# Optimization experiments

Measured on AMD Instinct MI355X. Metric: run time of the kernel, lower is better.

## Reference

```python
import jax, jax.numpy as jnp
import numpy as np

B, S, H, NH = 8, 1024, 1024, 16
D = H // NH          # attention_hidden_size = 64
V = S                # v_size must equal seq_len (mask broadcast)


def setup_inputs() -> dict:
    key = jax.random.key(0)
    ks = jax.random.split(key, 9)
    s = 0.02
    return {
        "q": jax.random.normal(ks[0], (B, S, H), jnp.float32),
        "k": jax.random.normal(ks[1], (B, S, H), jnp.float32),
        "v": jax.random.normal(ks[2], (B, S, H), jnp.float32),
        # per-head Q/K projections, stacked over heads: (NH, H, D)
        "Wq": jax.random.normal(ks[3], (NH, H, D), jnp.float32) * s,
        "bq": jax.random.normal(ks[4], (NH, D), jnp.float32) * s,
        "Wk": jax.random.normal(ks[5], (NH, H, D), jnp.float32) * s,
        "bk": jax.random.normal(ks[6], (NH, D), jnp.float32) * s,
        # shared V projection hidden -> v_size
        "Wv": jax.random.normal(ks[7], (H, V), jnp.float32) * s,
        "bv": jax.random.normal(ks[8], (V,), jnp.float32) * s,
    }


def reference(q, k, v, Wq, bq, Wk, bk, Wv, bv):
    d = Wq.shape[-1]
    scale = d ** (-0.5)
    # per-head projections, heads vectorized into leading axis n
    qh = jnp.einsum('bsh,nhd->nbsd', q, Wq) + bq[:, None, None, :]
    kh = jnp.einsum('bth,nhd->nbtd', k, Wk) + bk[:, None, None, :]
    vv = jnp.einsum('bth,hv->btv', v, Wv) + bv          # shared V: (B,S,V)
    seq = q.shape[1]
    mask = jnp.triu(jnp.full((seq, seq), -jnp.inf, dtype=q.dtype), 1)
    scores = jnp.einsum('nbsd,nbtd->nbst', qh, kh) * scale + mask
    p = jax.nn.softmax(scores, axis=-1)                  # (NH,B,S,S)
    # matmul against shared V then mean over heads (== stack + mean)
    out = jnp.einsum('nbst,btv->nbsv', p, vv).mean(axis=0)
    return out
```

## Files before the change

### kernel.cpp

```cpp
#include <hip/hip_runtime.h>


#define NHEAD 16
#define BATCH 8
#define SEQ   1024
#define HID   1024
#define DHEAD 64

typedef _Float16 f16;
typedef _Float16 f16x4 __attribute__((ext_vector_type(4)));
typedef _Float16 f16x8 __attribute__((ext_vector_type(8)));
typedef float    f32x4 __attribute__((ext_vector_type(4)));

__device__ __forceinline__ f32x4 mfma16(f16x8 a, f16x8 b, f32x4 c) {
  return __builtin_amdgcn_mfma_f32_16x16x32_f16(a, b, c, 0, 0, 0);
}

__device__ __forceinline__ void gload16(const f16* g, f16* l) {
  __builtin_amdgcn_global_load_lds(
      (const __attribute__((address_space(1))) void*)g,
      (__attribute__((address_space(3))) void*)l, 16, 0, 0);
}

__device__ __forceinline__ void stage_swz(const f16* __restrict__ g, int ldg,
                                          f16* lds, int nch, int tid) {
  for (int idx = tid; idx < nch; idx += 256) {
    int row = idx >> 3, c16 = idx & 7;
    int sc = c16 ^ (row & 7);
    gload16(g + (size_t)row * ldg + sc * 8, lds + (size_t)(idx & ~63) * 8);
  }
}

__device__ __forceinline__ f16x8 lds_frag(const f16* lds, int row, int c16) {
  int sc = c16 ^ (row & 7);
  return *(const f16x8*)&lds[row * 64 + sc * 8];
}


__global__ __launch_bounds__(256) void conv3(
    const float* __restrict__ q, const float* __restrict__ k,
    const float* __restrict__ v, f16* __restrict__ dq, f16* __restrict__ dk,
    f16* __restrict__ dv) {
  const float* src = blockIdx.z == 0 ? q : blockIdx.z == 1 ? k : v;
  f16* dst = blockIdx.z == 0 ? dq : blockIdx.z == 1 ? dk : dv;
  int i = (blockIdx.x * 256 + threadIdx.x) * 4;
  float4 f = *(const float4*)(src + i);
  f16x4 o = { (f16)f.x, (f16)f.y, (f16)f.z, (f16)f.w };
  *(f16x4*)(dst + i) = o;
}

__global__ __launch_bounds__(256) void tconv2(
    const float* __restrict__ s0, const float* __restrict__ s1,
    f16* __restrict__ d0, f16* __restrict__ d1, int R, int C, int half) {
  int z = blockIdx.z;
  const float* src; f16* dst;
  if (z < half) { src = s0 + (size_t)z * R * C; dst = d0 + (size_t)z * R * C; }
  else { src = s1 + (size_t)(z - half) * R * C; dst = d1 + (size_t)(z - half) * R * C; }
  const int c0 = blockIdx.x * 64, r0 = blockIdx.y * 64;
  __shared__ f16 t[64][72];
  const int tid = threadIdx.x;
#pragma unroll
  for (int i = 0; i < 4; i++) {
    int chunk = tid + i * 256;
    int row = chunk >> 4, c4 = chunk & 15;
    float4 f = *(const float4*)&src[(size_t)(r0 + row) * C + c0 + c4 * 4];
    f16x4 h = { (f16)f.x, (f16)f.y, (f16)f.z, (f16)f.w };
    *(f16x4*)&t[row][c4 * 4] = h;
  }
  __syncthreads();
  const int cc = tid >> 2, q = tid & 3;
  f16 tmp[16];
#pragma unroll
  for (int j = 0; j < 16; j++) tmp[j] = t[q * 16 + j][cc];
  *(f16x8*)&dst[(size_t)(c0 + cc) * R + r0 + q * 16] = *(f16x8*)&tmp[0];
  *(f16x8*)&dst[(size_t)(c0 + cc) * R + r0 + q * 16 + 8] = *(f16x8*)&tmp[8];
}


__device__ __forceinline__ void gemm_core(
    const f16* __restrict__ A, const f16* __restrict__ Bt, int K, int Kend,
    int row0, int col0, f16* la, f16* lb, int tid, f32x4 (&acc)[4][4]) {
  const int lane = tid & 63;
  const int wr = (tid >> 6) >> 1, wc = (tid >> 6) & 1;
  for (int k0 = 0; k0 < Kend; k0 += 64) {
    __syncthreads();
    stage_swz(A + (size_t)row0 * K + k0, K, la, 1024, tid);
    stage_swz(Bt + (size_t)col0 * K + k0, K, lb, 1024, tid);
    __syncthreads();
#pragma unroll
    for (int ks = 0; ks < 2; ks++) {
      f16x8 af[4], bfr[4];
#pragma unroll
      for (int mi = 0; mi < 4; mi++)
        af[mi] = lds_frag(la, wr * 64 + mi * 16 + (lane & 15), ks * 4 + (lane >> 4));
#pragma unroll
      for (int ni = 0; ni < 4; ni++)
        bfr[ni] = lds_frag(lb, wc * 64 + ni * 16 + (lane & 15), ks * 4 + (lane >> 4));
#pragma unroll
      for (int mi = 0; mi < 4; mi++)
#pragma unroll
        for (int ni = 0; ni < 4; ni++)
          acc[mi][ni] = mfma16(af[mi], bfr[ni], acc[mi][ni]);
    }
  }
}


__global__ __launch_bounds__(256) void proj_gemm(
    const f16* __restrict__ A0, const f16* __restrict__ A1,
    const f16* __restrict__ Bt0, const f16* __restrict__ Bt1,
    const float* __restrict__ bias0, const float* __restrict__ bias1,
    f16* __restrict__ C0, f16* __restrict__ C1) {
  const int which = blockIdx.z;
  const f16* A = which ? A1 : A0;
  const f16* Bt = which ? Bt1 : Bt0;
  const float* bias = which ? bias1 : bias0;
  f16* C = which ? C1 : C0;
  __shared__ alignas(16) f16 la[128 * 64];
  __shared__ alignas(16) f16 lb[128 * 64];
  const int tid = threadIdx.x, lane = tid & 63;
  const int wr = (tid >> 6) >> 1, wc = (tid >> 6) & 1;
  const int row0 = blockIdx.x * 128, col0 = blockIdx.y * 128;
  f32x4 acc[4][4];
#pragma unroll
  for (int i = 0; i < 4; i++)
#pragma unroll
    for (int j = 0; j < 4; j++) acc[i][j] = (f32x4){0.f, 0.f, 0.f, 0.f};
  gemm_core(A, Bt, HID, HID, row0, col0, la, lb, tid, acc);
#pragma unroll
  for (int mi = 0; mi < 4; mi++)
#pragma unroll
    for (int ni = 0; ni < 4; ni++)
#pragma unroll
      for (int r = 0; r < 4; r++) {
        int m = row0 + wr * 64 + mi * 16 + ((lane >> 4) << 2) + r;
        int j = col0 + wc * 64 + ni * 16 + (lane & 15);
        float val = acc[mi][ni][r] + bias[j];
        int bb = m >> 10, s = m & 1023, hn = j >> 6, d = j & 63;
        C[(((size_t)hn * BATCH + bb) * SEQ + s) * DHEAD + d] = (f16)val;
      }
}


__global__ __launch_bounds__(256) void vv_gemm(
    const f16* __restrict__ A, const f16* __restrict__ Bt,
    const float* __restrict__ bias, f16* __restrict__ C) {
  __shared__ alignas(16) f16 la[128 * 64];
  __shared__ alignas(16) f16 lb[128 * 64];
  const int tid = threadIdx.x, lane = tid & 63;
  const int wr = (tid >> 6) >> 1, wc = (tid >> 6) & 1;
  const int row0 = blockIdx.x * 128, col0 = blockIdx.y * 128;
  f32x4 acc[4][4];
#pragma unroll
  for (int i = 0; i < 4; i++)
#pragma unroll
    for (int j = 0; j < 4; j++) acc[i][j] = (f32x4){0.f, 0.f, 0.f, 0.f};
  gemm_core(A, Bt, HID, HID, row0, col0, la, lb, tid, acc);
#pragma unroll
  for (int mi = 0; mi < 4; mi++)
#pragma unroll
    for (int ni = 0; ni < 4; ni++)
#pragma unroll
      for (int r = 0; r < 4; r++) {
        int m = row0 + wr * 64 + mi * 16 + ((lane >> 4) << 2) + r;
        int j = col0 + wc * 64 + ni * 16 + (lane & 15);
        float val = acc[mi][ni][r] + bias[m];
        int bb = j >> 10, t = j & 1023;
        C[((size_t)bb * SEQ + m) * SEQ + t] = (f16)val;
      }
}


__global__ __launch_bounds__(256) void attn_stats(
    const f16* __restrict__ QH, const f16* __restrict__ KH,
    float* __restrict__ madj_ws) {
  const int flat = blockIdx.x;
  const int sb = 15 - (flat >> 7);
  const int nb = flat & 127;
  const int n = nb >> 3, b = nb & 7;
  const int s0 = sb * 64;
  const f16* qh = QH + ((size_t)n * BATCH + b) * SEQ * DHEAD;
  const f16* kh = KH + ((size_t)n * BATCH + b) * SEQ * DHEAD;

  const int tid = threadIdx.x, lane = tid & 63, wave = tid >> 6;
  const int lr = lane & 15;
  const int qg = lane >> 4;
  const int ch = qg << 3;

  f16x8 aq[4][2];
#pragma unroll
  for (int fi = 0; fi < 4; fi++) {
    const f16* qp = qh + (size_t)(s0 + fi * 16 + lr) * 64 + ch;
    aq[fi][0] = *(const f16x8*)qp;
    aq[fi][1] = *(const f16x8*)(qp + 32);
  }

  const float sl2e = 0.125f * 1.44269504088896f;
  float l_p[16];
#pragma unroll
  for (int i = 0; i < 16; i++) l_p[i] = 0.f;

  const int nt = (sb + 1) * 4;
  const int dstart = sb * 4;
  const int njw = (nt - wave + 3) >> 2;
  const f16* kp = kh + (size_t)lr * 64 + ch;

  f16x8 kA0, kA1, kB0, kB1;

#define LDK(jj, X0, X1) { const f16* p_ = kp + (size_t)(jj) * 1024; \
    X0 = *(const f16x8*)p_; X1 = *(const f16x8*)(p_ + 32); }

#define COMP(jj, X0, X1) { \
    f32x4 c_[4]; \
    _Pragma("unroll") for (int fi = 0; fi < 4; fi++) { \
      f32x4 cc = (f32x4){0.f, 0.f, 0.f, 0.f}; \
      cc = mfma16(aq[fi][0], X0, cc); cc = mfma16(aq[fi][1], X1, cc); \
      c_[fi] = cc; } \
    if ((jj) < dstart) { \
      _Pragma("unroll") for (int fi = 0; fi < 4; fi++) \
        _Pragma("unroll") for (int r = 0; r < 4; r++) \
          l_p[fi * 4 + r] += exp2f(c_[fi][r] * sl2e); \
    } else { \
      int tg_ = (jj) * 16 + lr; \
      _Pragma("unroll") for (int fi = 0; fi < 4; fi++) \
        _Pragma("unroll") for (int r = 0; r < 4; r++) { \
          int sg_ = s0 + fi * 16 + qg * 4 + r; \
          l_p[fi * 4 + r] += (tg_ <= sg_) ? exp2f(c_[fi][r] * sl2e) : 0.f; } } }

  LDK(wave, kA0, kA1);
  int idx = 0;
  for (; idx + 2 <= njw; idx += 2) {
    LDK(wave + (idx + 1) * 4, kB0, kB1);
    COMP(wave + idx * 4, kA0, kA1);
    if (idx + 2 < njw) LDK(wave + (idx + 2) * 4, kA0, kA1);
    COMP(wave + (idx + 1) * 4, kB0, kB1);
  }
  if (idx < njw) COMP(wave + idx * 4, kA0, kA1);
#undef LDK
#undef COMP

  __shared__ float lds_l[4][64];
#pragma unroll
  for (int i = 0; i < 16; i++) {
    float l = l_p[i];
    l += __shfl_xor(l, 1); l += __shfl_xor(l, 2);
    l += __shfl_xor(l, 4); l += __shfl_xor(l, 8);
    if (lr == 0) lds_l[wave][(i >> 2) * 16 + qg * 4 + (i & 3)] = l;
  }
  __syncthreads();
  if (tid < 64) {
    float l = lds_l[0][tid] + lds_l[1][tid] + lds_l[2][tid] + lds_l[3][tid];
    madj_ws[((size_t)n * BATCH + b) * SEQ + s0 + tid] = -__log2f(l) - 4.0f;
  }
}


__global__ __launch_bounds__(256) void pbar_gemm(
    const f16* __restrict__ QH, const f16* __restrict__ KH,
    const float* __restrict__ madj_ws, f16* __restrict__ pp) {
  int ti = blockIdx.x, rb = 0, cb = 0;
  {
    int t = ti;
#pragma unroll
    for (int r = 0; r < 8; ++r) {
      if (t <= r) { rb = r; cb = t; break; }
      t -= r + 1;
    }
  }
  const int r0 = rb * 128, c0 = cb * 128;
  const int y = blockIdx.y;
  const int b = y >> 1, g = y & 1;
  const int n0 = g * 8;
  const bool diag = (rb == cb);

  __shared__ alignas(16) f16 la[128 * 64];
  __shared__ alignas(16) f16 lb[128 * 64];

  const int tid = threadIdx.x, lane = tid & 63;
  const int wr = (tid >> 6) >> 1, wc = (tid >> 6) & 1;
  const int lr = lane & 15, qg = lane >> 4;
  const float sl2e = 0.125f * 1.44269504088896f;

  f32x4 pacc[4][4];
#pragma unroll
  for (int i = 0; i < 4; i++)
#pragma unroll
    for (int j = 0; j < 4; j++) pacc[i][j] = (f32x4){0.f, 0.f, 0.f, 0.f};

  for (int h = 0; h < 8; ++h) {
    const int n = n0 + h;
    const f16* qh = QH + ((size_t)n * BATCH + b) * SEQ * DHEAD;
    const f16* kh = KH + ((size_t)n * BATCH + b) * SEQ * DHEAD;

    __syncthreads();
    stage_swz(qh + (size_t)r0 * 64, 64, la, 1024, tid);
    stage_swz(kh + (size_t)c0 * 64, 64, lb, 1024, tid);
    __syncthreads();

    f32x4 acc[4][4];
#pragma unroll
    for (int i = 0; i < 4; i++)
#pragma unroll
      for (int j = 0; j < 4; j++) acc[i][j] = (f32x4){0.f, 0.f, 0.f, 0.f};

#pragma unroll
    for (int ks = 0; ks < 2; ks++) {
      f16x8 af[4], bfr[4];
#pragma unroll
      for (int mi = 0; mi < 4; mi++)
        af[mi] = lds_frag(la, wr * 64 + mi * 16 + lr, ks * 4 + qg);
#pragma unroll
      for (int ni = 0; ni < 4; ni++)
        bfr[ni] = lds_frag(lb, wc * 64 + ni * 16 + lr, ks * 4 + qg);
#pragma unroll
      for (int mi = 0; mi < 4; mi++)
#pragma unroll
        for (int ni = 0; ni < 4; ni++)
          acc[mi][ni] = mfma16(af[mi], bfr[ni], acc[mi][ni]);
    }

    const float* mb = madj_ws + ((size_t)n * BATCH + b) * SEQ + r0 +
                      wr * 64 + qg * 4;
#pragma unroll
    for (int mi = 0; mi < 4; mi++) {
      float4 m4 = *(const float4*)(mb + mi * 16);
      float ma[4] = {m4.x, m4.y, m4.z, m4.w};
#pragma unroll
      for (int ni = 0; ni < 4; ni++) {
        int tg = c0 + wc * 64 + ni * 16 + lr;
#pragma unroll
        for (int r = 0; r < 4; r++) {
          float p = exp2f(fmaf(acc[mi][ni][r], sl2e, ma[r]));
          if (diag) {
            int sg = r0 + wr * 64 + mi * 16 + qg * 4 + r;
            p = (tg <= sg) ? p : 0.f;
          }
          pacc[mi][ni][r] += p;
        }
      }
    }
  }

  f16* out = pp + ((size_t)g * BATCH + b) * SEQ * SEQ;
#pragma unroll
  for (int mi = 0; mi < 4; mi++)
#pragma unroll
    for (int ni = 0; ni < 4; ni++)
#pragma unroll
      for (int r = 0; r < 4; r++) {
        int m = r0 + wr * 64 + mi * 16 + qg * 4 + r;
        int j = c0 + wc * 64 + ni * 16 + lr;
        out[(size_t)m * SEQ + j] = (f16)pacc[mi][ni][r];
      }
}


__global__ __launch_bounds__(256) void pv_gemm(
    const f16* __restrict__ pp, const f16* __restrict__ vvT,
    float* __restrict__ out) {
  const int b = blockIdx.z;
  const size_t GS = (size_t)BATCH * SEQ * SEQ;
  const f16* A0 = pp + (size_t)b * SEQ * SEQ;
  const f16* A1 = pp + GS + (size_t)b * SEQ * SEQ;
  const f16* Bt = vvT + (size_t)b * SEQ * SEQ;
  __shared__ alignas(16) f16 la0[128 * 64];
  __shared__ alignas(16) f16 la1[128 * 64];
  __shared__ alignas(16) f16 lb[128 * 64];
  const int tid = threadIdx.x, lane = tid & 63;
  const int wr = (tid >> 6) >> 1, wc = (tid >> 6) & 1;
  const int row0 = blockIdx.x * 128, col0 = blockIdx.y * 128;
  const int Kend = (row0 + 128 < SEQ) ? row0 + 128 : SEQ;

  f32x4 acc[4][4];
#pragma unroll
  for (int i = 0; i < 4; i++)
#pragma unroll
    for (int j = 0; j < 4; j++) acc[i][j] = (f32x4){0.f, 0.f, 0.f, 0.f};

  for (int k0 = 0; k0 < Kend; k0 += 64) {
    __syncthreads();
    stage_swz(A0 + (size_t)row0 * SEQ + k0, SEQ, la0, 1024, tid);
    stage_swz(A1 + (size_t)row0 * SEQ + k0, SEQ, la1, 1024, tid);
    stage_swz(Bt + (size_t)col0 * SEQ + k0, SEQ, lb, 1024, tid);
    __syncthreads();
#pragma unroll
    for (int ks = 0; ks < 2; ks++) {
      f16x8 a0[4], a1[4], bfr[4];
#pragma unroll
      for (int mi = 0; mi < 4; mi++) {
        a0[mi] = lds_frag(la0, wr * 64 + mi * 16 + (lane & 15), ks * 4 + (lane >> 4));
        a1[mi] = lds_frag(la1, wr * 64 + mi * 16 + (lane & 15), ks * 4 + (lane >> 4));
      }
#pragma unroll
      for (int ni = 0; ni < 4; ni++)
        bfr[ni] = lds_frag(lb, wc * 64 + ni * 16 + (lane & 15), ks * 4 + (lane >> 4));
#pragma unroll
      for (int mi = 0; mi < 4; mi++)
#pragma unroll
        for (int ni = 0; ni < 4; ni++) {
          acc[mi][ni] = mfma16(a0[mi], bfr[ni], acc[mi][ni]);
          acc[mi][ni] = mfma16(a1[mi], bfr[ni], acc[mi][ni]);
        }
    }
  }

#pragma unroll
  for (int mi = 0; mi < 4; mi++)
#pragma unroll
    for (int ni = 0; ni < 4; ni++)
#pragma unroll
      for (int r = 0; r < 4; r++) {
        int m = row0 + wr * 64 + mi * 16 + ((lane >> 4) << 2) + r;
        int j = col0 + wc * 64 + ni * 16 + (lane & 15);
        out[(size_t)b * SEQ * SEQ + (size_t)m * SEQ + j] = acc[mi][ni][r];
      }
}


extern "C" void kernel_launch(void* const* d_in, const int* in_sizes, int n_in,
                              void* d_out, int out_size, void* d_ws, size_t ws_size,
                              hipStream_t stream) {
  (void)in_sizes; (void)n_in; (void)out_size; (void)ws_size;
  const float* q  = (const float*)d_in[0];
  const float* k  = (const float*)d_in[1];
  const float* v  = (const float*)d_in[2];
  const float* Wq = (const float*)d_in[3];
  const float* bq = (const float*)d_in[4];
  const float* Wk = (const float*)d_in[5];
  const float* bk = (const float*)d_in[6];
  const float* Wv = (const float*)d_in[7];
  const float* bv = (const float*)d_in[8];
  float* out = (float*)d_out;

  const size_t EL  = (size_t)BATCH * SEQ * HID;
  const size_t WEL = (size_t)NHEAD * HID * DHEAD;

  char* ws = (char*)d_ws;
  f16* qbf = (f16*)ws;  ws += EL * 2;
  f16* kbf = (f16*)ws;  ws += EL * 2;
  f16* vbf = (f16*)ws;  ws += EL * 2;
  f16* WqT = (f16*)ws;  ws += WEL * 2;
  f16* WkT = (f16*)ws;  ws += WEL * 2;
  f16* WvT = (f16*)ws;  ws += WEL * 2;
  f16* QHb = (f16*)ws;  ws += EL * 2;
  f16* KHb = (f16*)ws;  ws += EL * 2;
  f16* vvT = (f16*)ws;  ws += EL * 2;
  float* madj_ws = (float*)ws; ws += (size_t)NHEAD * BATCH * SEQ * 4;
  f16* pp = qbf;

  conv3<<<dim3(8192, 1, 3), 256, 0, stream>>>(q, k, v, qbf, kbf, vbf);
  tconv2<<<dim3(1, 16, 32), 256, 0, stream>>>(Wq, Wk, WqT, WkT, 1024, 64, 16);
  tconv2<<<dim3(16, 16, 1), 256, 0, stream>>>(Wv, Wv, WvT, WvT, 1024, 1024, 1);

  proj_gemm<<<dim3(64, 8, 2), 256, 0, stream>>>(qbf, kbf, WqT, WkT, bq, bk,
                                                QHb, KHb);
  vv_gemm<<<dim3(8, 64, 1), 256, 0, stream>>>(WvT, vbf, bv, vvT);

  attn_stats<<<dim3(2048, 1, 1), 256, 0, stream>>>(QHb, KHb, madj_ws);
  pbar_gemm<<<dim3(36, 16, 1), 256, 0, stream>>>(QHb, KHb, madj_ws, pp);
  pv_gemm<<<dim3(8, 8, 8), 256, 0, stream>>>(pp, vvT, out);
}
```

Measured before the change: 238.3 us.

## Double-buffer head tiles in pbar_gemm and remap blocks across XCDs

Gives pbar_gemm two LDS buffers for the Q/K head tiles so the load for the next head is issued while the current head's MFMAs and exp run. This removes one barrier per head and hides global-load latency. It also hoists the madj loads ahead of the compute and launches a flat 1D grid whose index is permuted so that consecutive blocks (same batch and group) land on the same XCD for L2 reuse. In exchange LDS use doubles to 64KB per block, which may lower occupancy.

```diff
diff --git a/kernel.cpp b/kernel.cpp
--- a/kernel.cpp
+++ b/kernel.cpp
@@ -258,9 +258,12 @@
 __global__ __launch_bounds__(256) void pbar_gemm(
     const f16* __restrict__ QH, const f16* __restrict__ KH,
     const float* __restrict__ madj_ws, f16* __restrict__ pp) {
-  int ti = blockIdx.x, rb = 0, cb = 0;
+  const int flat = blockIdx.x;
+  const int wg = (flat & 7) * 72 + (flat >> 3);
+  const int y = wg / 36;
+  int rb = 0, cb = 0;
   {
-    int t = ti;
+    int t = wg % 36;
 #pragma unroll
     for (int r = 0; r < 8; ++r) {
       if (t <= r) { rb = r; cb = t; break; }
@@ -268,18 +271,22 @@
     }
   }
   const int r0 = rb * 128, c0 = cb * 128;
-  const int y = blockIdx.y;
   const int b = y >> 1, g = y & 1;
   const int n0 = g * 8;
   const bool diag = (rb == cb);
 
-  __shared__ alignas(16) f16 la[128 * 64];
-  __shared__ alignas(16) f16 lb[128 * 64];
+  __shared__ alignas(16) f16 la[2][128 * 64];
+  __shared__ alignas(16) f16 lb[2][128 * 64];
 
   const int tid = threadIdx.x, lane = tid & 63;
   const int wr = (tid >> 6) >> 1, wc = (tid >> 6) & 1;
   const int lr = lane & 15, qg = lane >> 4;
   const float sl2e = 0.125f * 1.44269504088896f;
+  const size_t HS = (size_t)BATCH * SEQ * DHEAD;
+  const f16* qbase = QH + ((size_t)n0 * BATCH + b) * SEQ * DHEAD + (size_t)r0 * 64;
+  const f16* kbase = KH + ((size_t)n0 * BATCH + b) * SEQ * DHEAD + (size_t)c0 * 64;
+  const float* mbase = madj_ws + ((size_t)n0 * BATCH + b) * SEQ + r0 +
+                       wr * 64 + qg * 4;
 
   f32x4 pacc[4][4];
 #pragma unroll
@@ -287,15 +294,20 @@
 #pragma unroll
     for (int j = 0; j < 4; j++) pacc[i][j] = (f32x4){0.f, 0.f, 0.f, 0.f};
 
+  stage_swz(qbase, 64, la[0], 1024, tid);
+  stage_swz(kbase, 64, lb[0], 1024, tid);
+  __syncthreads();
+
   for (int h = 0; h < 8; ++h) {
-    const int n = n0 + h;
-    const f16* qh = QH + ((size_t)n * BATCH + b) * SEQ * DHEAD;
-    const f16* kh = KH + ((size_t)n * BATCH + b) * SEQ * DHEAD;
-
-    __syncthreads();
-    stage_swz(qh + (size_t)r0 * 64, 64, la, 1024, tid);
-    stage_swz(kh + (size_t)c0 * 64, 64, lb, 1024, tid);
-    __syncthreads();
+    const int cur = h & 1;
+    if (h + 1 < 8) {
+      stage_swz(qbase + (size_t)(h + 1) * HS, 64, la[cur ^ 1], 1024, tid);
+      stage_swz(kbase + (size_t)(h + 1) * HS, 64, lb[cur ^ 1], 1024, tid);
+    }
+    const float* mb = mbase + (size_t)h * BATCH * SEQ;
+    float4 m4[4];
+#pragma unroll
+    for (int mi = 0; mi < 4; mi++) m4[mi] = *(const float4*)(mb + mi * 16);
 
     f32x4 acc[4][4];
 #pragma unroll
@@ -308,10 +320,10 @@
       f16x8 af[4], bfr[4];
 #pragma unroll
       for (int mi = 0; mi < 4; mi++)
-        af[mi] = lds_frag(la, wr * 64 + mi * 16 + lr, ks * 4 + qg);
+        af[mi] = lds_frag(la[cur], wr * 64 + mi * 16 + lr, ks * 4 + qg);
 #pragma unroll
       for (int ni = 0; ni < 4; ni++)
-        bfr[ni] = lds_frag(lb, wc * 64 + ni * 16 + lr, ks * 4 + qg);
+        bfr[ni] = lds_frag(lb[cur], wc * 64 + ni * 16 + lr, ks * 4 + qg);
 #pragma unroll
       for (int mi = 0; mi < 4; mi++)
 #pragma unroll
@@ -319,12 +331,9 @@
           acc[mi][ni] = mfma16(af[mi], bfr[ni], acc[mi][ni]);
     }
 
-    const float* mb = madj_ws + ((size_t)n * BATCH + b) * SEQ + r0 +
-                      wr * 64 + qg * 4;
 #pragma unroll
     for (int mi = 0; mi < 4; mi++) {
-      float4 m4 = *(const float4*)(mb + mi * 16);
-      float ma[4] = {m4.x, m4.y, m4.z, m4.w};
+      float ma[4] = {m4[mi].x, m4[mi].y, m4[mi].z, m4[mi].w};
 #pragma unroll
       for (int ni = 0; ni < 4; ni++) {
         int tg = c0 + wc * 64 + ni * 16 + lr;
@@ -339,6 +348,7 @@
         }
       }
     }
+    __syncthreads();
   }
 
   f16* out = pp + ((size_t)g * BATCH + b) * SEQ * SEQ;
@@ -457,6 +467,6 @@
   vv_gemm<<<dim3(8, 64, 1), 256, 0, stream>>>(WvT, vbf, bv, vvT);
 
   attn_stats<<<dim3(2048, 1, 1), 256, 0, stream>>>(QHb, KHb, madj_ws);
-  pbar_gemm<<<dim3(36, 16, 1), 256, 0, stream>>>(QHb, KHb, madj_ws, pp);
+  pbar_gemm<<<dim3(576, 1, 1), 256, 0, stream>>>(QHb, KHb, madj_ws, pp);
   pv_gemm<<<dim3(8, 8, 8), 256, 0, stream>>>(pp, vvT, out);
 }
```

After: 227.9 us. 4.4% less time.
